# Kernel tuning notes

Hardware: AMD Instinct MI355X
Metric: run time of the kernel (lower is better)

The kernel has to match this reference:

```python
import jax, jax.numpy as jnp
import numpy as np

N_VERTEX = 16384
D_IN = 64
HIDDEN = 64
D_OUT = 8
N_REGIONS = 64


def setup_inputs() -> dict:
    key = jax.random.key(0)
    ks = jax.random.split(key, 16)
    h = jax.random.normal(ks[0], (N_VERTEX, D_IN), dtype=jnp.float32)
    norm_adj = jax.random.uniform(ks[1], (N_VERTEX, N_VERTEX), dtype=jnp.float32) / N_VERTEX
    region_index = jax.random.randint(ks[2], (N_VERTEX,), 0, N_REGIONS, dtype=jnp.int32)
    s = 1.0 / np.sqrt(D_IN)
    W1 = jax.random.normal(ks[3], (D_IN, HIDDEN), dtype=jnp.float32) * s
    L1 = jax.random.normal(ks[4], (D_IN, HIDDEN), dtype=jnp.float32) * s
    rw1 = jax.random.normal(ks[5], (N_REGIONS, HIDDEN), dtype=jnp.float32) * 0.1 + 1.0
    rb1 = jax.random.normal(ks[6], (N_REGIONS, HIDDEN), dtype=jnp.float32) * 0.1
    sh = 1.0 / np.sqrt(HIDDEN)
    W2 = jax.random.normal(ks[7], (HIDDEN, HIDDEN), dtype=jnp.float32) * sh
    L2 = jax.random.normal(ks[8], (HIDDEN, HIDDEN), dtype=jnp.float32) * sh
    rw2 = jax.random.normal(ks[9], (N_REGIONS, HIDDEN), dtype=jnp.float32) * 0.1 + 1.0
    rb2 = jax.random.normal(ks[10], (N_REGIONS, HIDDEN), dtype=jnp.float32) * 0.1
    Wout = jax.random.normal(ks[11], (D_OUT, HIDDEN), dtype=jnp.float32) * sh
    bout = jax.random.normal(ks[12], (D_OUT,), dtype=jnp.float32) * 0.1
    return dict(h=h, norm_adj=norm_adj, region_index=region_index,
                W1=W1, L1=L1, rw1=rw1, rb1=rb1,
                W2=W2, L2=L2, rw2=rw2, rb2=rb2,
                Wout=Wout, bout=bout)


def _reg_conv(h, norm_adj, region_index, W, L, reg_w, reg_b):
    # ra = h @ W ; rb = norm_adj @ (h @ L)   [N, d_out]
    z = h @ W + norm_adj @ (h @ L)
    # per-vertex region gather of affine params (the irregular-access hot path)
    return z * reg_w[region_index] + reg_b[region_index]


def reference(h, norm_adj, region_index, W1, L1, rw1, rb1, W2, L2, rw2, rb2, Wout, bout):
    x = jax.nn.relu(_reg_conv(h, norm_adj, region_index, W1, L1, rw1, rb1))
    x = jax.nn.relu(_reg_conv(x, norm_adj, region_index, W2, L2, rw2, rb2))
    return x @ Wout.T + bout  # [N, d_out]
```

## Files before the change

kernel.cpp:

```cpp
#include <hip/hip_runtime.h>
#include <stdint.h>

#define NV 16384
#define DH 64
#define BTS (NV + 64)
#define BK 256
#define LDST 264
#define NCH 32

typedef __attribute__((ext_vector_type(4))) float f32x4;
typedef __attribute__((ext_vector_type(8))) short s16x8;

static __device__ __forceinline__ unsigned short f2bf(float f) {
  union { float f; unsigned u; } x; x.f = f;
  unsigned r = x.u + 0x7fffu + ((x.u >> 16) & 1u);
  return (unsigned short)(r >> 16);
}

static __device__ __forceinline__ s16x8 cvt8(f32x4 a, f32x4 b) {
  s16x8 r;
  r[0] = (short)f2bf(a[0]); r[1] = (short)f2bf(a[1]);
  r[2] = (short)f2bf(a[2]); r[3] = (short)f2bf(a[3]);
  r[4] = (short)f2bf(b[0]); r[5] = (short)f2bf(b[1]);
  r[6] = (short)f2bf(b[2]); r[7] = (short)f2bf(b[3]);
  return r;
}

__global__ __launch_bounds__(256) void k_prep(
    const float* __restrict__ h, const float* __restrict__ W1,
    const float* __restrict__ L1, float* __restrict__ Z,
    unsigned short* __restrict__ Bt) {
  __shared__ float Ws[4096], Ls[4096], hs[16 * 64];
  int tid = threadIdx.x;
  for (int i = tid; i < 4096; i += 256) { Ws[i] = W1[i]; Ls[i] = L1[i]; }
  int r = tid >> 6, c = tid & 63;
  int i0 = blockIdx.x << 4;
  #pragma unroll
  for (int m = 0; m < 4; ++m)
    hs[(r + 4 * m) * 64 + c] = h[(size_t)(i0 + r + 4 * m) * 64 + c];
  __syncthreads();
  float a1[4] = {0.f, 0.f, 0.f, 0.f};
  float a2[4] = {0.f, 0.f, 0.f, 0.f};
  #pragma unroll 8
  for (int k = 0; k < 64; ++k) {
    float wv = Ws[k * 64 + c];
    float lv = Ls[k * 64 + c];
    #pragma unroll
    for (int m = 0; m < 4; ++m) {
      float hv = hs[(r + 4 * m) * 64 + k];
      a1[m] += hv * wv;
      a2[m] += hv * lv;
    }
  }
  #pragma unroll
  for (int m = 0; m < 4; ++m) {
    int i = i0 + r + 4 * m;
    Z[(size_t)i * 64 + c] = a1[m];
    Bt[(size_t)c * BTS + i] = f2bf(a2[m]);
  }
}

__global__ __launch_bounds__(256, 2) void k_adj(
    const float* __restrict__ adj, const unsigned short* __restrict__ Bt,
    float* __restrict__ P) {
  __shared__ __align__(16) unsigned short Blds[2 * 64 * LDST];
  const int tid = threadIdx.x;
  const int lane = tid & 63;
  const int w = tid >> 6;
  const int l15 = lane & 15;
  const int kgrp = lane >> 4;
  const int xb = blockIdx.x;
  const int yb = blockIdx.y;
  const int row = (xb << 6) + (w << 4) + l15;
  const int kbase = yb << 13;

  const int srow = tid >> 4;
  const int sc16 = tid & 15;
  const unsigned short* sbase = Bt + (size_t)srow * BTS + kbase + sc16 * 8;
  unsigned short* lbase = Blds + srow * LDST + sc16 * 8;

  const float* ap = adj + (size_t)row * NV + kbase + kgrp * 8;
  const int bofs0 = (l15 +  0) * LDST + kgrp * 8;
  const int bofs1 = (l15 + 16) * LDST + kgrp * 8;
  const int bofs2 = (l15 + 32) * LDST + kgrp * 8;
  const int bofs3 = (l15 + 48) * LDST + kgrp * 8;

  f32x4 sr0, sr1, sr2, sr3, sr4, sr5, sr6, sr7;
#define STAGE_LOAD(KC)                                                   \
  { const unsigned short* s_ = sbase + (KC);                             \
    sr0 = *(const f32x4*)(s_);                                           \
    sr1 = *(const f32x4*)(s_ + 128);                                     \
    sr2 = *(const f32x4*)(s_ + (size_t)16 * BTS);                        \
    sr3 = *(const f32x4*)(s_ + (size_t)16 * BTS + 128);                  \
    sr4 = *(const f32x4*)(s_ + (size_t)32 * BTS);                        \
    sr5 = *(const f32x4*)(s_ + (size_t)32 * BTS + 128);                  \
    sr6 = *(const f32x4*)(s_ + (size_t)48 * BTS);                        \
    sr7 = *(const f32x4*)(s_ + (size_t)48 * BTS + 128); }
#define STAGE_WRITE(BUF)                                                 \
  { unsigned short* d_ = lbase + (BUF) * (64 * LDST);                    \
    *(f32x4*)(d_) = sr0;                                                 \
    *(f32x4*)(d_ + 128) = sr1;                                           \
    *(f32x4*)(d_ + 16 * LDST) = sr2;                                     \
    *(f32x4*)(d_ + 16 * LDST + 128) = sr3;                               \
    *(f32x4*)(d_ + 32 * LDST) = sr4;                                     \
    *(f32x4*)(d_ + 32 * LDST + 128) = sr5;                               \
    *(f32x4*)(d_ + 48 * LDST) = sr6;                                     \
    *(f32x4*)(d_ + 48 * LDST + 128) = sr7; }

  f32x4 aj0a, aj0b, aj1a, aj1b, aj2a, aj2b, aj3a, aj3b;

  STAGE_LOAD(0);
  aj0a = *(const f32x4*)(ap +   0); aj0b = *(const f32x4*)(ap +   4);
  aj1a = *(const f32x4*)(ap +  32); aj1b = *(const f32x4*)(ap +  36);
  aj2a = *(const f32x4*)(ap +  64); aj2b = *(const f32x4*)(ap +  68);
  aj3a = *(const f32x4*)(ap +  96); aj3b = *(const f32x4*)(ap + 100);
  STAGE_WRITE(0);
  __syncthreads();

  f32x4 acc0 = {0.f, 0.f, 0.f, 0.f};
  f32x4 acc1 = {0.f, 0.f, 0.f, 0.f};
  f32x4 acc2 = {0.f, 0.f, 0.f, 0.f};
  f32x4 acc3 = {0.f, 0.f, 0.f, 0.f};

#define ITER(II, AJA, AJB)                                               \
  {                                                                      \
    s16x8 af = cvt8(AJA, AJB);                                           \
    int ci = ((t << 3) + (II) + 4) & 255;                                \
    AJA = *(const f32x4*)(ap + (size_t)ci * 32);                         \
    AJB = *(const f32x4*)(ap + (size_t)ci * 32 + 4);                     \
    s16x8 cb0 = *(const s16x8*)(bb + bofs0 + (II) * 32);                 \
    s16x8 cb1 = *(const s16x8*)(bb + bofs1 + (II) * 32);                 \
    s16x8 cb2 = *(const s16x8*)(bb + bofs2 + (II) * 32);                 \
    s16x8 cb3 = *(const s16x8*)(bb + bofs3 + (II) * 32);                 \
    acc0 = __builtin_amdgcn_mfma_f32_16x16x32_bf16(af, cb0, acc0, 0, 0, 0); \
    acc1 = __builtin_amdgcn_mfma_f32_16x16x32_bf16(af, cb1, acc1, 0, 0, 0); \
    acc2 = __builtin_amdgcn_mfma_f32_16x16x32_bf16(af, cb2, acc2, 0, 0, 0); \
    acc3 = __builtin_amdgcn_mfma_f32_16x16x32_bf16(af, cb3, acc3, 0, 0, 0); \
  }

  for (int t = 0; t < NCH; ++t) {
    const unsigned short* bb = Blds + (t & 1) * (64 * LDST);
    if (t + 1 < NCH) STAGE_LOAD((t + 1) * BK);
    ITER(0, aj0a, aj0b)
    ITER(1, aj1a, aj1b)
    ITER(2, aj2a, aj2b)
    ITER(3, aj3a, aj3b)
    ITER(4, aj0a, aj0b)
    ITER(5, aj1a, aj1b)
    ITER(6, aj2a, aj2b)
    ITER(7, aj3a, aj3b)
    if (t + 1 < NCH) STAGE_WRITE((t + 1) & 1);
    __syncthreads();
  }

  int zr = (xb << 6) + (w << 4) + (kgrp << 2);
  float* pp = P + (size_t)yb * NV * 64 + (size_t)zr * 64 + l15;
  #pragma unroll
  for (int r = 0; r < 4; ++r) {
    pp[(size_t)r * 64 +  0] = acc0[r];
    pp[(size_t)r * 64 + 16] = acc1[r];
    pp[(size_t)r * 64 + 32] = acc2[r];
    pp[(size_t)r * 64 + 48] = acc3[r];
  }
#undef STAGE_LOAD
#undef STAGE_WRITE
#undef ITER
}

__global__ __launch_bounds__(256) void k_mid(
    float* __restrict__ Z, const float* __restrict__ P,
    const int* __restrict__ reg,
    const float* __restrict__ rw1, const float* __restrict__ rb1,
    const float* __restrict__ W2, const float* __restrict__ L2,
    unsigned short* __restrict__ Bt) {
  __shared__ float Ws[4096], Ls[4096], xs[16 * 64];
  int tid = threadIdx.x;
  for (int i = tid; i < 4096; i += 256) { Ws[i] = W2[i]; Ls[i] = L2[i]; }
  int r = tid >> 6, c = tid & 63;
  int i0 = blockIdx.x << 4;
  #pragma unroll
  for (int m = 0; m < 4; ++m) {
    int i = i0 + r + 4 * m;
    int ri = reg[i];
    size_t o = (size_t)i * 64 + c;
    float z = Z[o] + P[o] + P[(size_t)NV * 64 + o];
    float x = z * rw1[ri * 64 + c] + rb1[ri * 64 + c];
    xs[(r + 4 * m) * 64 + c] = fmaxf(x, 0.f);
  }
  __syncthreads();
  float a1[4] = {0.f, 0.f, 0.f, 0.f};
  float a2[4] = {0.f, 0.f, 0.f, 0.f};
  #pragma unroll 8
  for (int k = 0; k < 64; ++k) {
    float wv = Ws[k * 64 + c];
    float lv = Ls[k * 64 + c];
    #pragma unroll
    for (int m = 0; m < 4; ++m) {
      float xv = xs[(r + 4 * m) * 64 + k];
      a1[m] += xv * wv;
      a2[m] += xv * lv;
    }
  }
  #pragma unroll
  for (int m = 0; m < 4; ++m) {
    int i = i0 + r + 4 * m;
    Z[(size_t)i * 64 + c] = a1[m];
    Bt[(size_t)c * BTS + i] = f2bf(a2[m]);
  }
}

__global__ __launch_bounds__(256) void k_out(
    const float* __restrict__ Z, const float* __restrict__ P,
    const int* __restrict__ reg,
    const float* __restrict__ rw2, const float* __restrict__ rb2,
    const float* __restrict__ Wout, const float* __restrict__ bout,
    float* __restrict__ out) {
  __shared__ float xs[16 * 64];
  int tid = threadIdx.x;
  int r = tid >> 6, c = tid & 63;
  int i0 = blockIdx.x << 4;
  #pragma unroll
  for (int m = 0; m < 4; ++m) {
    int i = i0 + r + 4 * m;
    int ri = reg[i];
    size_t o = (size_t)i * 64 + c;
    float z = Z[o] + P[o] + P[(size_t)NV * 64 + o];
    float x = z * rw2[ri * 64 + c] + rb2[ri * 64 + c];
    xs[(r + 4 * m) * 64 + c] = fmaxf(x, 0.f);
  }
  __syncthreads();
  if (c < 8) {
    #pragma unroll
    for (int m = 0; m < 4; ++m) {
      int i = i0 + r + 4 * m;
      float a = bout[c];
      #pragma unroll 8
      for (int k = 0; k < 64; ++k) a += xs[(r + 4 * m) * 64 + k] * Wout[c * 64 + k];
      out[(size_t)i * 8 + c] = a;
    }
  }
}

extern "C" void kernel_launch(void* const* d_in, const int* in_sizes, int n_in,
                              void* d_out, int out_size, void* d_ws, size_t ws_size,
                              hipStream_t stream) {
  const float* h    = (const float*)d_in[0];
  const float* adj  = (const float*)d_in[1];
  const int*   reg  = (const int*)d_in[2];
  const float* W1   = (const float*)d_in[3];
  const float* L1   = (const float*)d_in[4];
  const float* rw1  = (const float*)d_in[5];
  const float* rb1  = (const float*)d_in[6];
  const float* W2   = (const float*)d_in[7];
  const float* L2   = (const float*)d_in[8];
  const float* rw2  = (const float*)d_in[9];
  const float* rb2  = (const float*)d_in[10];
  const float* Wout = (const float*)d_in[11];
  const float* bout = (const float*)d_in[12];
  float* out = (float*)d_out;

  float* Z = (float*)d_ws;
  unsigned short* Bt = (unsigned short*)((char*)d_ws + ((size_t)4 << 20));
  float* P = (float*)((char*)d_ws + ((size_t)8 << 20));

  k_prep<<<NV / 16, 256, 0, stream>>>(h, W1, L1, Z, Bt);
  k_adj<<<dim3(NV / 64, 2), 256, 0, stream>>>(adj, Bt, P);
  k_mid<<<NV / 16, 256, 0, stream>>>(Z, P, reg, rw1, rb1, W2, L2, Bt);
  k_adj<<<dim3(NV / 64, 2), 256, 0, stream>>>(adj, Bt, P);
  k_out<<<NV / 16, 256, 0, stream>>>(Z, P, reg, rw2, rb2, Wout, bout, out);
}
```

Baseline: 433.9 us.

## Cache fp8-quantized adjacency in first pass and run second adjacency GEMM in fp8

The first adjacency GEMM now also writes a scaled fp8 copy of the adjacency matrix to workspace, and the second layer's GEMM reads that 1-byte copy with fp8 MFMA instead of re-reading the fp32 adjacency. The aim is to cut the dominant HBM traffic of the second pass by about a factor of four and use the faster fp8 matrix instructions. In exchange, the first pass pays an extra write stream of 256MB, and accuracy drops from fp8 quantization of both the adjacency and the hidden features. The hidden features are quantized without scaling, which risks precision loss.

Result: slower. 515.2 us (+18.7%).

```diff
diff --git a/kernel.cpp b/kernel.cpp
--- a/kernel.cpp
+++ b/kernel.cpp
@@ -4,9 +4,13 @@
 #define NV 16384
 #define DH 64
 #define BTS (NV + 64)
+#define BTQS (NV + 64)
 #define BK 256
 #define LDST 264
+#define LDST8 272
 #define NCH 32
+#define SCUP 16384.0f
+#define SCDN 6.103515625e-05f
 
 typedef __attribute__((ext_vector_type(4))) float f32x4;
 typedef __attribute__((ext_vector_type(8))) short s16x8;
@@ -62,7 +66,7 @@
 
 __global__ __launch_bounds__(256, 2) void k_adj(
     const float* __restrict__ adj, const unsigned short* __restrict__ Bt,
-    float* __restrict__ P) {
+    float* __restrict__ P, unsigned char* __restrict__ adj8) {
   __shared__ __align__(16) unsigned short Blds[2 * 64 * LDST];
   const int tid = threadIdx.x;
   const int lane = tid & 63;
@@ -80,6 +84,7 @@
   unsigned short* lbase = Blds + srow * LDST + sc16 * 8;
 
   const float* ap = adj + (size_t)row * NV + kbase + kgrp * 8;
+  unsigned char* a8 = adj8 + (size_t)row * NV + kbase + kgrp * 8;
   const int bofs0 = (l15 +  0) * LDST + kgrp * 8;
   const int bofs1 = (l15 + 16) * LDST + kgrp * 8;
   const int bofs2 = (l15 + 32) * LDST + kgrp * 8;
@@ -125,6 +130,12 @@
 #define ITER(II, AJA, AJB)                                               \
   {                                                                      \
     s16x8 af = cvt8(AJA, AJB);                                           \
+    unsigned pk0 = __builtin_amdgcn_cvt_pk_fp8_f32(AJA[0] * SCUP, AJA[1] * SCUP, 0, false); \
+    pk0 = __builtin_amdgcn_cvt_pk_fp8_f32(AJA[2] * SCUP, AJA[3] * SCUP, pk0, true);         \
+    unsigned pk1 = __builtin_amdgcn_cvt_pk_fp8_f32(AJB[0] * SCUP, AJB[1] * SCUP, 0, false); \
+    pk1 = __builtin_amdgcn_cvt_pk_fp8_f32(AJB[2] * SCUP, AJB[3] * SCUP, pk1, true);         \
+    *(unsigned long long*)(a8 + (size_t)(((t << 3) + (II)) * 32)) =      \
+        (unsigned long long)pk0 | ((unsigned long long)pk1 << 32);       \
     int ci = ((t << 3) + (II) + 4) & 255;                                \
     AJA = *(const f32x4*)(ap + (size_t)ci * 32);                         \
     AJB = *(const f32x4*)(ap + (size_t)ci * 32 + 4);                     \
@@ -167,12 +178,110 @@
 #undef ITER
 }
 
+__global__ __launch_bounds__(256, 2) void k_adj8(
+    const unsigned char* __restrict__ adj8, const unsigned char* __restrict__ Btq,
+    float* __restrict__ P) {
+  __shared__ __align__(16) unsigned char Blds[2 * 64 * LDST8];
+  const int tid = threadIdx.x;
+  const int lane = tid & 63;
+  const int w = tid >> 6;
+  const int l15 = lane & 15;
+  const int kgrp = lane >> 4;
+  const int xb = blockIdx.x;
+  const int yb = blockIdx.y;
+  const int row = (xb << 6) + (w << 4) + l15;
+  const int kbase = yb << 13;
+
+  const int srow = tid >> 4;
+  const int sc16 = tid & 15;
+  const unsigned char* sbase = Btq + (size_t)srow * BTQS + kbase + sc16 * 16;
+  unsigned char* lbase = Blds + srow * LDST8 + sc16 * 16;
+
+  const unsigned char* ap8 = adj8 + (size_t)row * NV + kbase + kgrp * 8;
+  const int bofs0 = (l15 +  0) * LDST8 + kgrp * 8;
+  const int bofs1 = (l15 + 16) * LDST8 + kgrp * 8;
+  const int bofs2 = (l15 + 32) * LDST8 + kgrp * 8;
+  const int bofs3 = (l15 + 48) * LDST8 + kgrp * 8;
+
+  f32x4 sr0, sr1, sr2, sr3;
+#define STAGE_LOAD8(KC)                                                  \
+  { const unsigned char* s_ = sbase + (KC);                              \
+    sr0 = *(const f32x4*)(s_);                                           \
+    sr1 = *(const f32x4*)(s_ + (size_t)16 * BTQS);                       \
+    sr2 = *(const f32x4*)(s_ + (size_t)32 * BTQS);                       \
+    sr3 = *(const f32x4*)(s_ + (size_t)48 * BTQS); }
+#define STAGE_WRITE8(BUF)                                                \
+  { unsigned char* d_ = lbase + (BUF) * (64 * LDST8);                    \
+    *(f32x4*)(d_) = sr0;                                                 \
+    *(f32x4*)(d_ + 16 * LDST8) = sr1;                                    \
+    *(f32x4*)(d_ + 32 * LDST8) = sr2;                                    \
+    *(f32x4*)(d_ + 48 * LDST8) = sr3; }
+
+  unsigned long long aj0, aj1, aj2, aj3;
+
+  STAGE_LOAD8(0);
+  aj0 = *(const unsigned long long*)(ap8 +  0);
+  aj1 = *(const unsigned long long*)(ap8 + 32);
+  aj2 = *(const unsigned long long*)(ap8 + 64);
+  aj3 = *(const unsigned long long*)(ap8 + 96);
+  STAGE_WRITE8(0);
+  __syncthreads();
+
+  f32x4 acc0 = {0.f, 0.f, 0.f, 0.f};
+  f32x4 acc1 = {0.f, 0.f, 0.f, 0.f};
+  f32x4 acc2 = {0.f, 0.f, 0.f, 0.f};
+  f32x4 acc3 = {0.f, 0.f, 0.f, 0.f};
+
+#define ITER8(II, AJ)                                                    \
+  {                                                                      \
+    long long a_ = (long long)AJ;                                        \
+    int ci = ((t << 3) + (II) + 4) & 255;                                \
+    AJ = *(const unsigned long long*)(ap8 + (size_t)ci * 32);            \
+    long long b0 = *(const long long*)(bb + bofs0 + (II) * 32);          \
+    long long b1 = *(const long long*)(bb + bofs1 + (II) * 32);          \
+    long long b2 = *(const long long*)(bb + bofs2 + (II) * 32);          \
+    long long b3 = *(const long long*)(bb + bofs3 + (II) * 32);          \
+    acc0 = __builtin_amdgcn_mfma_f32_16x16x32_fp8_fp8(a_, b0, acc0, 0, 0, 0); \
+    acc1 = __builtin_amdgcn_mfma_f32_16x16x32_fp8_fp8(a_, b1, acc1, 0, 0, 0); \
+    acc2 = __builtin_amdgcn_mfma_f32_16x16x32_fp8_fp8(a_, b2, acc2, 0, 0, 0); \
+    acc3 = __builtin_amdgcn_mfma_f32_16x16x32_fp8_fp8(a_, b3, acc3, 0, 0, 0); \
+  }
+
+  for (int t = 0; t < NCH; ++t) {
+    const unsigned char* bb = Blds + (t & 1) * (64 * LDST8);
+    if (t + 1 < NCH) STAGE_LOAD8((t + 1) * BK);
+    ITER8(0, aj0)
+    ITER8(1, aj1)
+    ITER8(2, aj2)
+    ITER8(3, aj3)
+    ITER8(4, aj0)
+    ITER8(5, aj1)
+    ITER8(6, aj2)
+    ITER8(7, aj3)
+    if (t + 1 < NCH) STAGE_WRITE8((t + 1) & 1);
+    __syncthreads();
+  }
+
+  int zr = (xb << 6) + (w << 4) + (kgrp << 2);
+  float* pp = P + (size_t)yb * NV * 64 + (size_t)zr * 64 + l15;
+  #pragma unroll
+  for (int r = 0; r < 4; ++r) {
+    pp[(size_t)r * 64 +  0] = acc0[r] * SCDN;
+    pp[(size_t)r * 64 + 16] = acc1[r] * SCDN;
+    pp[(size_t)r * 64 + 32] = acc2[r] * SCDN;
+    pp[(size_t)r * 64 + 48] = acc3[r] * SCDN;
+  }
+#undef STAGE_LOAD8
+#undef STAGE_WRITE8
+#undef ITER8
+}
+
 __global__ __launch_bounds__(256) void k_mid(
     float* __restrict__ Z, const float* __restrict__ P,
     const int* __restrict__ reg,
     const float* __restrict__ rw1, const float* __restrict__ rb1,
     const float* __restrict__ W2, const float* __restrict__ L2,
-    unsigned short* __restrict__ Bt) {
+    unsigned char* __restrict__ Btq) {
   __shared__ float Ws[4096], Ls[4096], xs[16 * 64];
   int tid = threadIdx.x;
   for (int i = tid; i < 4096; i += 256) { Ws[i] = W2[i]; Ls[i] = L2[i]; }
@@ -205,7 +314,8 @@
   for (int m = 0; m < 4; ++m) {
     int i = i0 + r + 4 * m;
     Z[(size_t)i * 64 + c] = a1[m];
-    Bt[(size_t)c * BTS + i] = f2bf(a2[m]);
+    unsigned q = __builtin_amdgcn_cvt_pk_fp8_f32(a2[m], 0.0f, 0, false);
+    Btq[(size_t)c * BTQS + i] = (unsigned char)(q & 0xff);
   }
 }
 
@@ -259,13 +369,16 @@
   const float* bout = (const float*)d_in[12];
   float* out = (float*)d_out;
 
-  float* Z = (float*)d_ws;
-  unsigned short* Bt = (unsigned short*)((char*)d_ws + ((size_t)4 << 20));
-  float* P = (float*)((char*)d_ws + ((size_t)8 << 20));
+  char* ws = (char*)d_ws;
+  float* Z            = (float*)(ws);
+  unsigned short* Bt  = (unsigned short*)(ws + ((size_t)4  << 20));
+  float* P            = (float*)(ws + ((size_t)8  << 20));
+  unsigned char* Btq  = (unsigned char*)(ws + ((size_t)16 << 20));
+  unsigned char* adj8 = (unsigned char*)(ws + ((size_t)20 << 20));
 
   k_prep<<<NV / 16, 256, 0, stream>>>(h, W1, L1, Z, Bt);
-  k_adj<<<dim3(NV / 64, 2), 256, 0, stream>>>(adj, Bt, P);
-  k_mid<<<NV / 16, 256, 0, stream>>>(Z, P, reg, rw1, rb1, W2, L2, Bt);
-  k_adj<<<dim3(NV / 64, 2), 256, 0, stream>>>(adj, Bt, P);
+  k_adj<<<dim3(NV / 64, 2), 256, 0, stream>>>(adj, Bt, P, adj8);
+  k_mid<<<NV / 16, 256, 0, stream>>>(Z, P, reg, rw1, rb1, W2, L2, Btq);
+  k_adj8<<<dim3(NV / 64, 2), 256, 0, stream>>>(adj8, Btq, P);
   k_out<<<NV / 16, 256, 0, stream>>>(Z, P, reg, rw2, rb2, Wout, bout, out);
 }
```
